# Optimization experiments

Measured on AMD Instinct MI355X. Metric: run time of the kernel, lower is better.

The kernel has to match this reference:

```python
import jax, jax.numpy as jnp
import numpy as np

B, S, D, H = 4, 2048, 1024, 16
HD = D // H

def setup_inputs() -> dict:
    key = jax.random.key(0)
    k1, k2, k3, k4, k5 = jax.random.split(key, 5)
    sc = 1.0 / np.sqrt(D)
    return {
        "x": jax.random.normal(k1, (B, S, D), dtype=jnp.float32),
        "w_qkv": jax.random.normal(k2, (D, 3 * D), dtype=jnp.float32) * sc,
        "b_qkv": jnp.zeros((3 * D,), dtype=jnp.float32),
        "w_proj": jax.random.normal(k3, (D, D), dtype=jnp.float32) * sc,
        "b_proj": jnp.zeros((D,), dtype=jnp.float32),
    }

def reference(x, w_qkv, b_qkv, w_proj, b_proj):
    bsz, seq_len, dim = x.shape
    qkv = x @ w_qkv + b_qkv                      # [B,S,3D]
    q, k, v = jnp.split(qkv, 3, axis=2)
    q = q.reshape(bsz, seq_len, H, HD).transpose(0, 2, 1, 3)  # [B,H,S,hd]
    k = k.reshape(bsz, seq_len, H, HD).transpose(0, 2, 1, 3)
    v = v.reshape(bsz, seq_len, H, HD).transpose(0, 2, 1, 3)
    att = jnp.einsum('bhqd,bhkd->bhqk', q, k) * (1.0 / np.sqrt(HD))
    causal = jnp.tril(jnp.ones((seq_len, seq_len), dtype=bool))
    att = jnp.where(causal[None, None], att, -jnp.inf)
    att = jax.nn.softmax(att, axis=-1)
    y = jnp.einsum('bhqk,bhkd->bhqd', att, v)
    y = y.transpose(0, 2, 1, 3).reshape(bsz, seq_len, dim)
    return y @ w_proj + b_proj
```

## Files before the change

kernel.cpp:

```cpp
#include <hip/hip_runtime.h>
#include <cstdint>
#include <cstddef>

typedef float  f32x4  __attribute__((ext_vector_type(4)));
typedef __bf16 bf16x8 __attribute__((ext_vector_type(8)));
typedef __bf16 bf16x4 __attribute__((ext_vector_type(4)));

#define DEVI static __device__ __forceinline__

DEVI f32x4 mfma_bf16(bf16x8 a, bf16x8 b, f32x4 c) {
  return __builtin_amdgcn_mfma_f32_16x16x32_bf16(a, b, c, 0, 0, 0);
}

DEVI void gload_lds16(const void* g, void* l) {
  __builtin_amdgcn_global_load_lds(
      (const __attribute__((address_space(1))) void*)g,
      (__attribute__((address_space(3))) void*)l, 16, 0, 0);
}

__global__ void k_cast_bf16(const float* __restrict__ src, __bf16* __restrict__ dst, int n4) {
  int i = blockIdx.x * blockDim.x + threadIdx.x;
  if (i < n4) {
    float4 v = reinterpret_cast<const float4*>(src)[i];
    bf16x4 r;
    r.x = (__bf16)v.x; r.y = (__bf16)v.y; r.z = (__bf16)v.z; r.w = (__bf16)v.w;
    reinterpret_cast<bf16x4*>(dst)[i] = r;
  }
}

__global__ void k_transpose_cast(const float* __restrict__ src, __bf16* __restrict__ dst,
                                 int R, int C) {
  __shared__ __bf16 tile[64][65];
  const int tx = threadIdx.x & 63, ty = threadIdx.x >> 6;
  const int r0 = blockIdx.y * 64, c0 = blockIdx.x * 64;
#pragma unroll
  for (int i = 0; i < 16; ++i) {
    int r = ty * 16 + i;
    tile[r][tx] = (__bf16)src[(size_t)(r0 + r) * C + c0 + tx];
  }
  __syncthreads();
#pragma unroll
  for (int i = 0; i < 16; ++i) {
    int c = ty * 16 + i;
    dst[(size_t)(c0 + c) * R + r0 + tx] = tile[tx][c];
  }
}

template <int MODE>
__global__ __launch_bounds__(256, 2) void k_gemm_bt(
    const __bf16* __restrict__ A, const __bf16* __restrict__ Bt,
    const float* __restrict__ bias, void* __restrict__ Cv,
    __bf16* __restrict__ VT,
    int M, int N, int K, int nbx) {
  __shared__ __bf16 As[128 * 64];
  __shared__ __bf16 Bs[128 * 64];
  const int t = threadIdx.x;
  const int w = t >> 6, lane = t & 63;
  const int l15 = lane & 15, lg = lane >> 4;
  const int m0 = (blockIdx.x / nbx) * 128;
  const int n0 = (blockIdx.x % nbx) * 128;
  const int wr = w >> 1, wc = w & 1;
  const int lrow = lane >> 3, lslot = lane & 7;

  f32x4 acc[4][4] = {};

  const int nK = K >> 6;
  for (int kt = 0; kt < nK; ++kt) {
    const __bf16* Ab = A + (size_t)m0 * K + kt * 64;
    const __bf16* Bb = Bt + (size_t)n0 * K + kt * 64;
#pragma unroll
    for (int c = 0; c < 4; ++c) {
      int seg = w * 4 + c;
      int row = seg * 8 + lrow;
      int cb = (lslot ^ (row & 7)) << 4;
      gload_lds16((const char*)(Ab + (size_t)row * K) + cb, (char*)As + seg * 1024);
      gload_lds16((const char*)(Bb + (size_t)row * K) + cb, (char*)Bs + seg * 1024);
    }
    __syncthreads();
#pragma unroll
    for (int ks = 0; ks < 2; ++ks) {
      bf16x8 af[4], bfr[4];
      const int cb = ks * 64 + (lg << 4);
#pragma unroll
      for (int m = 0; m < 4; ++m) {
        int row = wr * 64 + m * 16 + l15;
        af[m] = *(const bf16x8*)((const char*)As + row * 128 + (cb ^ ((row & 7) << 4)));
      }
#pragma unroll
      for (int n = 0; n < 4; ++n) {
        int row = wc * 64 + n * 16 + l15;
        bfr[n] = *(const bf16x8*)((const char*)Bs + row * 128 + (cb ^ ((row & 7) << 4)));
      }
#pragma unroll
      for (int m = 0; m < 4; ++m)
#pragma unroll
        for (int n = 0; n < 4; ++n)
          acc[m][n] = mfma_bf16(af[m], bfr[n], acc[m][n]);
    }
    __syncthreads();
  }

  const bool vsec = (MODE == 0) && (VT != nullptr) && (n0 >= 2048);
#pragma unroll
  for (int n = 0; n < 4; ++n) {
    const int gcol = n0 + wc * 64 + n * 16 + l15;
    const float bv = bias ? bias[gcol] : 0.0f;
#pragma unroll
    for (int m = 0; m < 4; ++m) {
      const int grow = m0 + wr * 64 + m * 16 + (lg << 2);
      if (vsec) {
        const int hd = gcol - 2048;
        const int b = grow >> 11, s0v = grow & 2047;
        const int nib = (s0v >> 2) & 15;
        const int nib2 = (nib < 4) ? 2 * nib : (nib < 8) ? 2 * nib - 7
                        : (nib < 12) ? 2 * nib - 8 : 2 * nib - 15;
        const int sp = (s0v & ~63) | (nib2 << 2);
        bf16x4 pkv;
#pragma unroll
        for (int r = 0; r < 4; ++r) pkv[r] = (__bf16)(acc[m][n][r] + bv);
        *(bf16x4*)(VT + ((size_t)(b * 16) * 64 + hd) * 2048 + sp) = pkv;
      } else {
#pragma unroll
        for (int r = 0; r < 4; ++r) {
          float v = acc[m][n][r] + bv;
          if (MODE == 0)
            ((__bf16*)Cv)[(size_t)(grow + r) * N + gcol] = (__bf16)v;
          else
            ((float*)Cv)[(size_t)(grow + r) * N + gcol] = v;
        }
      }
    }
  }
}

__global__ __launch_bounds__(512, 2) void k_attn(
    const __bf16* __restrict__ qkv,
    const __bf16* __restrict__ VT,
    __bf16* __restrict__ Y) {
  __shared__ __bf16 kbuf[2][64 * 64];
  __shared__ __bf16 vbuf[2][64 * 64];
  const int t = threadIdx.x, w = t >> 6, lane = t & 63;
  const int l15 = lane & 15, lg = lane >> 4;
  const int bid = blockIdx.x;
  const int qt = 15 - (bid >> 6);
  const int bh = bid & 63;
  const int b = bh >> 4, h = bh & 15;
  const int q0 = qt * 128;
  const int nkv = 2 * qt + 2;
  const float SCL = 0.125f * 1.44269504f;

  const size_t qrow = (size_t)(b * 2048 + q0 + w * 16 + l15);
  const bf16x8 qf0 = *(const bf16x8*)(qkv + qrow * 3072 + h * 64 + lg * 8);
  const bf16x8 qf1 = *(const bf16x8*)(qkv + qrow * 3072 + h * 64 + 32 + lg * 8);

  const __bf16* kg = qkv + (size_t)(b * 2048) * 3072 + 1024 + h * 64;
  const __bf16* vg = VT + (size_t)bh * 64 * 2048;

  const int srow = t >> 3, sslot = t & 7;
  const int sb = (sslot ^ (srow & 7)) << 4;
  auto stage = [&](int bi, int kvi) {
    gload_lds16((const char*)(kg + (size_t)(kvi * 64 + srow) * 3072) + sb,
                (char*)kbuf[bi] + w * 1024);
    gload_lds16((const char*)(vg + (size_t)srow * 2048 + kvi * 64) + sb,
                (char*)vbuf[bi] + w * 1024);
  };

  f32x4 o[4] = {};
  float mr = -1e30f, lr = 0.0f;

  stage(0, 0);
  asm volatile("s_waitcnt vmcnt(0)" ::: "memory");
  __syncthreads();

  for (int kv = 0; kv < nkv; ++kv) {
    if (kv + 1 < nkv) stage((kv + 1) & 1, kv + 1);
    const char* kb = (const char*)kbuf[kv & 1];
    const char* vb = (const char*)vbuf[kv & 1];

    f32x4 s[4] = {};
    __builtin_amdgcn_s_setprio(1);
#pragma unroll
    for (int nb = 0; nb < 4; ++nb) {
      int row = nb * 16 + l15;
      int sw = (row & 7) << 4;
      bf16x8 k0 = *(const bf16x8*)(kb + row * 128 + ((lg * 16) ^ sw));
      bf16x8 k1 = *(const bf16x8*)(kb + row * 128 + ((64 + lg * 16) ^ sw));
      s[nb] = mfma_bf16(k0, qf0, s[nb]);
      s[nb] = mfma_bf16(k1, qf1, s[nb]);
    }
    __builtin_amdgcn_s_setprio(0);

    if (((kv + 1) << 6) > q0 + w * 16) {
      const int qg = q0 + w * 16 + l15;
#pragma unroll
      for (int nb = 0; nb < 4; ++nb)
#pragma unroll
        for (int r = 0; r < 4; ++r)
          if (kv * 64 + nb * 16 + lg * 4 + r > qg) s[nb][r] = -1e30f;
    }

    float pm = -3e38f;
#pragma unroll
    for (int nb = 0; nb < 4; ++nb)
      pm = fmaxf(pm, fmaxf(fmaxf(s[nb][0], s[nb][1]), fmaxf(s[nb][2], s[nb][3])));
    pm = fmaxf(pm, __shfl_xor(pm, 16));
    pm = fmaxf(pm, __shfl_xor(pm, 32));
    pm *= SCL;

    if (!__all(pm <= mr + 8.0f)) {
      float nm = fmaxf(mr, pm);
      float alpha = __builtin_amdgcn_exp2f(mr - nm);
      lr *= alpha;
      mr = nm;
#pragma unroll
      for (int r = 0; r < 4; ++r) {
        float aO = __shfl(alpha, lg * 4 + r);
        o[0][r] *= aO; o[1][r] *= aO; o[2][r] *= aO; o[3][r] *= aO;
      }
    }

    float ps = 0.0f;
    bf16x4 pk[4];
#pragma unroll
    for (int nb = 0; nb < 4; ++nb) {
      f32x4 pe;
#pragma unroll
      for (int r = 0; r < 4; ++r)
        pe[r] = __builtin_amdgcn_exp2f(fmaf(s[nb][r], SCL, -mr));
      ps += (pe[0] + pe[1]) + (pe[2] + pe[3]);
      pk[nb][0] = (__bf16)pe[0]; pk[nb][1] = (__bf16)pe[1];
      pk[nb][2] = (__bf16)pe[2]; pk[nb][3] = (__bf16)pe[3];
    }
    ps += __shfl_xor(ps, 16);
    ps += __shfl_xor(ps, 32);
    lr += ps;

    const bf16x8 pf0 = __builtin_shufflevector(pk[0], pk[1], 0, 1, 2, 3, 4, 5, 6, 7);
    const bf16x8 pf1 = __builtin_shufflevector(pk[2], pk[3], 0, 1, 2, 3, 4, 5, 6, 7);
    __builtin_amdgcn_s_setprio(1);
#pragma unroll
    for (int nb = 0; nb < 4; ++nb) {
      int row = nb * 16 + l15;
      int sw = (row & 7) << 4;
      bf16x8 v0 = *(const bf16x8*)(vb + row * 128 + ((lg * 16) ^ sw));
      bf16x8 v1 = *(const bf16x8*)(vb + row * 128 + ((64 + lg * 16) ^ sw));
      o[nb] = mfma_bf16(pf0, v0, o[nb]);
      o[nb] = mfma_bf16(pf1, v1, o[nb]);
    }
    __builtin_amdgcn_s_setprio(0);
    asm volatile("s_waitcnt vmcnt(0)" ::: "memory");
    __syncthreads();
  }

  float lO[4];
#pragma unroll
  for (int r = 0; r < 4; ++r) lO[r] = __shfl(lr, lg * 4 + r);
#pragma unroll
  for (int nb = 0; nb < 4; ++nb)
#pragma unroll
    for (int r = 0; r < 4; ++r) {
      float v = o[nb][r] / lO[r];
      size_t row = (size_t)(b * 2048 + q0 + w * 16 + lg * 4 + r);
      Y[row * 1024 + h * 64 + nb * 16 + l15] = (__bf16)v;
    }
}

extern "C" void kernel_launch(void* const* d_in, const int* in_sizes, int n_in,
                              void* d_out, int out_size, void* d_ws, size_t ws_size,
                              hipStream_t stream) {
  const float* x      = (const float*)d_in[0];
  const float* w_qkv  = (const float*)d_in[1];
  const float* b_qkv  = (const float*)d_in[2];
  const float* w_proj = (const float*)d_in[3];
  const float* b_proj = (const float*)d_in[4];
  float* out = (float*)d_out;

  char* ws = (char*)d_ws;
  const size_t MB = 1024 * 1024;
  __bf16* xb     = (__bf16*)(ws);
  __bf16* wqkvT  = (__bf16*)(ws + 16 * MB);
  __bf16* wprojT = (__bf16*)(ws + 22 * MB);
  __bf16* qkv    = (__bf16*)(ws + 24 * MB);
  __bf16* VT     = (__bf16*)(ws + 72 * MB);
  __bf16* Y      = (__bf16*)(ws + 88 * MB);

  k_cast_bf16<<<8192, 256, 0, stream>>>(x, xb, 8192 * 1024 / 4);
  k_transpose_cast<<<dim3(48, 16), 256, 0, stream>>>(w_qkv, wqkvT, 1024, 3072);
  k_transpose_cast<<<dim3(16, 16), 256, 0, stream>>>(w_proj, wprojT, 1024, 1024);
  k_gemm_bt<0><<<dim3(64 * 24), 256, 0, stream>>>(xb, wqkvT, b_qkv, qkv, VT, 8192, 3072, 1024, 24);
  k_attn<<<dim3(1024), 512, 0, stream>>>(qkv, VT, Y);
  k_gemm_bt<1><<<dim3(64 * 8), 256, 0, stream>>>(Y, wprojT, b_proj, out, nullptr, 8192, 1024, 1024, 8);
}
```

Before: 171.2 us.

## Merge prep kernels, interleave attention q-tile order, flatten softmax max reduction

Replaces the three cast and transpose launches with one k_prep kernel that dispatches on block index, saving two launches and the gaps between them. Changes how attention blocks map to query tiles: long and short causal tiles now alternate in groups instead of running longest-first, which aims to balance load across CUs. Also rewrites the row-max reduction as a shallower tree to shorten the dependency chain. The new tile order may cause a worse tail than longest-first scheduling.

```diff
diff --git a/kernel.cpp b/kernel.cpp
--- a/kernel.cpp
+++ b/kernel.cpp
@@ -18,21 +18,30 @@
       (__attribute__((address_space(3))) void*)l, 16, 0, 0);
 }
 
-__global__ void k_cast_bf16(const float* __restrict__ src, __bf16* __restrict__ dst, int n4) {
-  int i = blockIdx.x * blockDim.x + threadIdx.x;
-  if (i < n4) {
-    float4 v = reinterpret_cast<const float4*>(src)[i];
+__global__ __launch_bounds__(256) void k_prep(
+    const float* __restrict__ x, __bf16* __restrict__ xb,
+    const float* __restrict__ w_qkv, __bf16* __restrict__ wqkvT,
+    const float* __restrict__ w_proj, __bf16* __restrict__ wprojT) {
+  __shared__ __bf16 tile[64][65];
+  const int idx = blockIdx.x;
+  if (idx < 8192) {
+    int i = idx * 256 + threadIdx.x;
+    float4 v = reinterpret_cast<const float4*>(x)[i];
     bf16x4 r;
     r.x = (__bf16)v.x; r.y = (__bf16)v.y; r.z = (__bf16)v.z; r.w = (__bf16)v.w;
-    reinterpret_cast<bf16x4*>(dst)[i] = r;
-  }
-}
-
-__global__ void k_transpose_cast(const float* __restrict__ src, __bf16* __restrict__ dst,
-                                 int R, int C) {
-  __shared__ __bf16 tile[64][65];
+    reinterpret_cast<bf16x4*>(xb)[i] = r;
+    return;
+  }
+  const float* src; __bf16* dst; int R, C, bx, by;
+  if (idx < 8960) {
+    int id2 = idx - 8192; bx = id2 % 48; by = id2 / 48;
+    src = w_qkv; dst = wqkvT; R = 1024; C = 3072;
+  } else {
+    int id2 = idx - 8960; bx = id2 % 16; by = id2 / 16;
+    src = w_proj; dst = wprojT; R = 1024; C = 1024;
+  }
   const int tx = threadIdx.x & 63, ty = threadIdx.x >> 6;
-  const int r0 = blockIdx.y * 64, c0 = blockIdx.x * 64;
+  const int r0 = by * 64, c0 = bx * 64;
 #pragma unroll
   for (int i = 0; i < 16; ++i) {
     int r = ty * 16 + i;
@@ -142,7 +151,8 @@
   const int t = threadIdx.x, w = t >> 6, lane = t & 63;
   const int l15 = lane & 15, lg = lane >> 4;
   const int bid = blockIdx.x;
-  const int qt = 15 - (bid >> 6);
+  const int g = bid >> 6;
+  const int qt = (g < 4) ? 15 - g : (g < 8) ? g - 4 : (g < 12) ? 19 - g : g - 8;
   const int bh = bid & 63;
   const int b = bh >> 4, h = bh & 15;
   const int q0 = qt * 128;
@@ -199,10 +209,12 @@
           if (kv * 64 + nb * 16 + lg * 4 + r > qg) s[nb][r] = -1e30f;
     }
 
-    float pm = -3e38f;
-#pragma unroll
-    for (int nb = 0; nb < 4; ++nb)
-      pm = fmaxf(pm, fmaxf(fmaxf(s[nb][0], s[nb][1]), fmaxf(s[nb][2], s[nb][3])));
+    float a0 = fmaxf(fmaxf(s[0][0], s[0][1]), s[0][2]);
+    float a1 = fmaxf(fmaxf(s[0][3], s[1][0]), s[1][1]);
+    float a2 = fmaxf(fmaxf(s[1][2], s[1][3]), s[2][0]);
+    float a3 = fmaxf(fmaxf(s[2][1], s[2][2]), s[2][3]);
+    float a4 = fmaxf(fmaxf(s[3][0], s[3][1]), s[3][2]);
+    float pm = fmaxf(fmaxf(fmaxf(a0, a1), a2), fmaxf(fmaxf(a3, a4), s[3][3]));
     pm = fmaxf(pm, __shfl_xor(pm, 16));
     pm = fmaxf(pm, __shfl_xor(pm, 32));
     pm *= SCL;
@@ -284,9 +296,7 @@
   __bf16* VT     = (__bf16*)(ws + 72 * MB);
   __bf16* Y      = (__bf16*)(ws + 88 * MB);
 
-  k_cast_bf16<<<8192, 256, 0, stream>>>(x, xb, 8192 * 1024 / 4);
-  k_transpose_cast<<<dim3(48, 16), 256, 0, stream>>>(w_qkv, wqkvT, 1024, 3072);
-  k_transpose_cast<<<dim3(16, 16), 256, 0, stream>>>(w_proj, wprojT, 1024, 1024);
+  k_prep<<<dim3(9216), 256, 0, stream>>>(x, xb, w_qkv, wqkvT, w_proj, wprojT);
   k_gemm_bt<0><<<dim3(64 * 24), 256, 0, stream>>>(xb, wqkvT, b_qkv, qkv, VT, 8192, 3072, 1024, 24);
   k_attn<<<dim3(1024), 512, 0, stream>>>(qkv, VT, Y);
   k_gemm_bt<1><<<dim3(64 * 8), 256, 0, stream>>>(Y, wprojT, b_proj, out, nullptr, 8192, 1024, 1024, 8);
```

After: 165.4 us. 1.04x faster.
